# Performance work log

Hardware: AMD Instinct MI355X
Metric: run time of the kernel (lower is better)

## Reference

```python
import jax, jax.numpy as jnp
import numpy as np

B = 512      # streamlines (graphs in the batch)
L = 128      # points per streamline
M = L - 1    # edges per direction per streamline == conv output length
IN = 3       # 3-D coordinates
K = 5        # kNN neighbors (self included, as in PyG knn)
FOV = 5      # conv kernel; odd so conv out length == M, matching the batch vector
PAD = FOV // 2
NC = 2
EPS = 1e-5


def _bn(x, g, b, m, v):
    # inference-mode BatchNorm1d
    return (x - m) * jax.lax.rsqrt(v + EPS) * g + b


def setup_inputs():
    key = jax.random.key(0)
    ks = jax.random.split(key, 20)
    r = lambda i, shape: jax.random.normal(ks[i], shape, jnp.float32) * 0.05
    ones = lambda n: jnp.ones((n,), jnp.float32)
    zeros = lambda n: jnp.zeros((n,), jnp.float32)
    pos = jax.random.normal(ks[0], (B * L, IN), jnp.float32)
    # consecutive-point (forward) edges, streamline-major order
    base = (jnp.arange(B)[:, None] * L + jnp.arange(M)[None, :]).reshape(-1)
    fwd = jnp.stack([base, base + 1]).astype(jnp.int32)          # [2, B*M]
    eidx = jnp.concatenate([fwd, fwd], axis=1)                   # [2, 2*B*M]; first half overwritten in forward
    batch = jnp.repeat(jnp.arange(B, dtype=jnp.int32), L)        # per-point graph id
    lengths = jnp.full((B,), L, dtype=jnp.int32)
    return dict(
        pos=pos, eidx=eidx, batch=batch, lengths=lengths,
        conv1_w=r(1, (FOV, 2 * IN, 64)), conv1_b=r(2, (64,)),
        bn1_g=ones(64), bn1_b=zeros(64), bn1_m=r(3, (64,)), bn1_v=ones(64),
        edge_w=r(4, (2 * 64, 128)), edge_b=r(5, (128,)),
        bn2_g=ones(128), bn2_b=zeros(128), bn2_m=r(6, (128,)), bn2_v=ones(128),
        lin1_w=r(7, (64 + 128, 1024)), lin1_b=r(8, (1024,)),
        bn3_g=ones(1024), bn3_b=zeros(1024), bn3_m=r(9, (1024,)), bn3_v=ones(1024),
        m1_w=r(10, (1024, 512)), m1_b=r(11, (512,)),
        bn4_g=ones(512), bn4_b=zeros(512), bn4_m=r(12, (512,)), bn4_v=ones(512),
        m2_w=r(13, (512, 256)), m2_b=r(14, (256,)),
        bn5_g=ones(256), bn5_b=zeros(256), bn5_m=r(15, (256,)), bn5_v=ones(256),
        out_w=r(16, (256, NC)), out_b=r(17, (NC,)),
    )


def reference(pos, eidx, batch, lengths,
              conv1_w, conv1_b, bn1_g, bn1_b, bn1_m, bn1_v,
              edge_w, edge_b, bn2_g, bn2_b, bn2_m, bn2_v,
              lin1_w, lin1_b, bn3_g, bn3_b, bn3_m, bn3_v,
              m1_w, m1_b, bn4_g, bn4_b, bn4_m, bn4_v,
              m2_w, m2_b, bn5_g, bn5_b, bn5_m, bn5_v,
              out_w, out_b):
    E = eidx.shape[1]
    half = eidx[:, E // 2:]
    # eidx[:, :E//2] = eidx[:, E//2:].flip(1)
    eidx = jnp.concatenate([half[:, ::-1], half], axis=1)
    # irregular gather: edge features [E, 2*IN]
    feats = jnp.concatenate([pos[eidx[1]] - pos[eidx[0]], pos[eidx[0]]], axis=1)
    x = feats.reshape(2 * B, M, 2 * IN)                            # folded direction+batch
    # Conv1d (cross-correlation) -> BN -> ReLU, channels-last layout
    x = jax.lax.conv_general_dilated(x, conv1_w, (1,), [(PAD, PAD)],
                                     dimension_numbers=('NWC', 'WIO', 'NWC')) + conv1_b
    x = jax.nn.relu(_bn(x, bn1_g, bn1_b, bn1_m, bn1_v))            # [2B, M, 64]
    # direction symmetrization: max(first half, second half flipped on batch & length)
    x = jnp.maximum(x[:B], x[B:][::-1, ::-1, :])                   # [B, M, 64]
    x1 = x.reshape(B * M, 64)
    # ---- DynamicEdgeConv: per-streamline kNN graph + edge MLP + max aggregation ----
    xg = x1.reshape(B, M, 64)
    sq = jnp.sum(xg * xg, axis=-1)                                 # [B, M]
    dist = sq[:, :, None] + sq[:, None, :] - 2.0 * jnp.einsum('bmd,bnd->bmn', xg, xg)
    _, idx = jax.lax.top_k(-dist, K)                               # [B, M, K] (self included)
    xj = jax.vmap(lambda xs, ix: xs[ix])(xg, idx)                  # [B, M, K, 64]
    xi = jnp.broadcast_to(xg[:, :, None, :], xj.shape)
    ef = jnp.concatenate([xi, xj - xi], axis=-1)                   # [B, M, K, 128]
    ef = _bn(jax.nn.relu(ef @ edge_w + edge_b), bn2_g, bn2_b, bn2_m, bn2_v)
    x2 = jnp.max(ef, axis=2).reshape(B * M, 128)                   # max aggr over neighbors
    # ---- lin1 + global max pool + classifier MLP (dropout = identity in eval) ----
    h = jnp.concatenate([x1, x2], axis=1)                          # [N, 192]
    h = _bn(jax.nn.relu(h @ lin1_w + lin1_b), bn3_g, bn3_b, bn3_m, bn3_v)  # [N, 1024]
    g = jnp.max(h.reshape(B, M, 1024), axis=1)                     # global_max_pool -> [B, 1024]
    g = _bn(jax.nn.relu(g @ m1_w + m1_b), bn4_g, bn4_b, bn4_m, bn4_v)
    g = _bn(jax.nn.relu(g @ m2_w + m2_b), bn5_g, bn5_b, bn5_m, bn5_v)
    return g @ out_w + out_b                                       # [B, NC]
```

## Files before the change

kernel.cpp:

```cpp
#include <hip/hip_runtime.h>

#define BB 512
#define LL 128
#define MM 127
#define EPS 1e-5f

typedef _Float16 half4 __attribute__((ext_vector_type(4)));
typedef _Float16 half8 __attribute__((ext_vector_type(8)));
typedef float f32x16 __attribute__((ext_vector_type(16)));

#define HB_PITCH 384
#define HB_BATCH 49152

__global__ __launch_bounds__(256) void k0_prep(
    const float* __restrict__ lw, char* __restrict__ lwT,
    const float* __restrict__ ew, char* __restrict__ ewT,
    const float* __restrict__ m1w, char* __restrict__ m1wT,
    const float* __restrict__ m2w, char* __restrict__ m2wT)
{
  int tid = threadIdx.x;
  __shared__ float ws2[256][32];
  if (blockIdx.x < 32) {
    int c0 = blockIdx.x * 32;
    __shared__ float wcol[192][32];
    for (int i = tid; i < 192 * 32; i += 256) {
      int k = i >> 5, c = i & 31;
      wcol[k][c] = lw[k * 1024 + c0 + c];
    }
    __syncthreads();
    for (int j = tid; j < 768; j += 256) {
      int kg = j >> 5, c = j & 31;
      half8 v;
#pragma unroll
      for (int jj = 0; jj < 8; jj++) v[jj] = (_Float16)wcol[kg * 8 + jj][c];
      int cc = c0 + c;
      *(half8*)(lwT + cc * HB_PITCH + ((kg * 16) ^ ((cc & 7) << 4))) = v;
    }
  } else if (blockIdx.x == 32) {
    __shared__ float es[128][128];
    for (int i = tid; i < 128 * 128; i += 256) es[i >> 7][i & 127] = ew[i];
    __syncthreads();
    for (int i = tid; i < 256 * 8; i += 256) {
      int c = i >> 3, kg = i & 7;
      half8 v;
#pragma unroll
      for (int jj = 0; jj < 8; jj++) {
        int k = kg * 8 + jj;
        float val = (c < 128) ? (es[k][c] - es[64 + k][c]) : es[64 + k][c - 128];
        v[jj] = (_Float16)val;
      }
      *(half8*)(ewT + c * 128 + ((kg * 16) ^ ((c & 7) << 4))) = v;
    }
  } else {
    const float* src; char* dst; int N, K, c0, k0;
    if (blockIdx.x < 97) {
      int bb = blockIdx.x - 33;
      src = m1w; dst = m1wT; N = 512; K = 1024;
      c0 = (bb >> 2) * 32; k0 = (bb & 3) * 256;
    } else {
      int bb = blockIdx.x - 97;
      src = m2w; dst = m2wT; N = 256; K = 512;
      c0 = (bb >> 1) * 32; k0 = (bb & 1) * 256;
    }
    for (int i = tid; i < 256 * 32; i += 256) {
      int k = i >> 5, c = i & 31;
      ws2[k][c] = src[(size_t)(k0 + k) * N + c0 + c];
    }
    __syncthreads();
    for (int j = tid; j < 32 * 32; j += 256) {
      int kg = j >> 5, c = j & 31;
      half8 v;
#pragma unroll
      for (int jj = 0; jj < 8; jj++) v[jj] = (_Float16)ws2[kg * 8 + jj][c];
      int cc = c0 + c;
      *(half8*)(dst + (size_t)cc * (2 * K) + ((2 * (k0 + kg * 8)) ^ ((cc & 7) << 4))) = v;
    }
  }
}

__global__ __launch_bounds__(256, 1) void k1_conv_knn(
    const float* __restrict__ pos, const float* __restrict__ cw,
    const float* __restrict__ cb, const float* __restrict__ g1,
    const float* __restrict__ b1, const float* __restrict__ m1,
    const float* __restrict__ v1, char* __restrict__ hb,
    int* __restrict__ idxb)
{
  int b = blockIdx.x;
  int tid = threadIdx.x;
  __shared__ float ps[LL * 3];
  __shared__ float fpad[MM + 4][6];
  __shared__ float ws[5 * 6 * 64];
  __shared__ float s1s[64], t1s[64];
  __shared__ float xs[128][64];
  __shared__ float sq[128];
  __shared__ float S[128][132];
  __shared__ float bsl[2][128][5];
  __shared__ int   bil[2][128][5];

  for (int i = tid; i < LL * 3; i += 256) ps[i] = pos[b * LL * 3 + i];
  for (int i = tid; i < 5 * 6 * 64; i += 256) ws[i] = cw[i];
  if (tid < 64) {
    float s = g1[tid] * rsqrtf(v1[tid] + EPS);
    s1s[tid] = s;
    t1s[tid] = (cb[tid] - m1[tid]) * s + b1[tid];
  }
  if (tid < 24) {
    int r = tid / 6, c = tid % 6;
    int rr = (r < 2) ? r : (MM + r);
    fpad[rr][c] = 0.f;
  }
  if (tid < 64) xs[127][tid] = 0.f;
  __syncthreads();
  for (int i = tid; i < MM * 6; i += 256) {
    int m = i / 6, c = i % 6;
    float v = (c < 3) ? (ps[(m + 1) * 3 + c] - ps[m * 3 + c]) : ps[m * 3 + c - 3];
    fpad[m + 2][c] = v;
  }
  __syncthreads();
  int orow = BB - 1 - b;
  char* hbb = hb + (size_t)orow * HB_BATCH;
  if (tid < 8) *(float4*)(hbb + 127 * HB_PITCH + tid * 16) = make_float4(0.f, 0.f, 0.f, 0.f);
  for (int o = tid; o < MM * 64; o += 256) {
    int m = o >> 6, c = o & 63;
    float af = 0.f, ab = 0.f;
#pragma unroll
    for (int t = 0; t < 5; t++) {
#pragma unroll
      for (int ci = 0; ci < 6; ci++) {
        float wv = ws[(t * 6 + ci) * 64 + c];
        af = fmaf(fpad[m + t][ci], wv, af);
        ab = fmaf(fpad[m + 4 - t][ci], wv, ab);
      }
    }
    float z = fmaxf(af, ab) * s1s[c] + t1s[c];
    float xv = fmaxf(z, 0.f);
    int p = MM - 1 - m;
    xs[p][(((c >> 2) + (p >> 3)) & 15) * 4 + (c & 3)] = xv;
    *(_Float16*)(hbb + p * HB_PITCH + ((2 * c) ^ ((p & 7) << 4))) = (_Float16)xv;
  }
  __syncthreads();
  if (tid < 128) {
    int r = tid;
    float s = 0.f;
#pragma unroll
    for (int c4 = 0; c4 < 16; c4++) {
      float4 v = *(const float4*)&xs[r][((c4 + (r >> 3)) & 15) * 4];
      s = fmaf(v.x, v.x, s); s = fmaf(v.y, v.y, s);
      s = fmaf(v.z, v.z, s); s = fmaf(v.w, v.w, s);
    }
    sq[r] = s;
  }
  __syncthreads();
  {
    int tr = tid >> 4, tc = tid & 15;
    float acc[8][8];
#pragma unroll
    for (int i = 0; i < 8; i++)
#pragma unroll
      for (int j = 0; j < 8; j++) acc[i][j] = 0.f;
    for (int k4 = 0; k4 < 16; k4++) {
      int ca = ((k4 + tr) & 15) * 4;
      int cbo = ((k4 + tc) & 15) * 4;
      float4 av[8], bv[8];
#pragma unroll
      for (int i = 0; i < 8; i++) av[i] = *(const float4*)&xs[tr * 8 + i][ca];
#pragma unroll
      for (int j = 0; j < 8; j++) bv[j] = *(const float4*)&xs[tc * 8 + j][cbo];
#pragma unroll
      for (int i = 0; i < 8; i++)
#pragma unroll
        for (int j = 0; j < 8; j++) {
          acc[i][j] = fmaf(av[i].x, bv[j].x, acc[i][j]);
          acc[i][j] = fmaf(av[i].y, bv[j].y, acc[i][j]);
          acc[i][j] = fmaf(av[i].z, bv[j].z, acc[i][j]);
          acc[i][j] = fmaf(av[i].w, bv[j].w, acc[i][j]);
        }
    }
    float sqc[8];
#pragma unroll
    for (int j = 0; j < 8; j++) sqc[j] = sq[tc * 8 + j];
#pragma unroll
    for (int i = 0; i < 8; i++) {
      float4 s0, s1;
      s0.x = sqc[0] - 2.f * acc[i][0]; s0.y = sqc[1] - 2.f * acc[i][1];
      s0.z = sqc[2] - 2.f * acc[i][2]; s0.w = sqc[3] - 2.f * acc[i][3];
      s1.x = sqc[4] - 2.f * acc[i][4]; s1.y = sqc[5] - 2.f * acc[i][5];
      s1.z = sqc[6] - 2.f * acc[i][6]; s1.w = sqc[7] - 2.f * acc[i][7];
      *(float4*)&S[tr * 8 + i][tc * 8]     = s0;
      *(float4*)&S[tr * 8 + i][tc * 8 + 4] = s1;
    }
  }
  __syncthreads();
  {
    int row = tid & 127, half = tid >> 7;
    float bs[5]; int bi[5];
#pragma unroll
    for (int k = 0; k < 5; k++) { bs[k] = 1e30f; bi[k] = 0; }
    for (int q = 0; q < 16; q++) {
      float4 sv = *(const float4*)&S[row][half * 64 + q * 4];
      int cbase = half * 64 + q * 4;
      float va[4] = {sv.x, sv.y, sv.z, sv.w};
#pragma unroll
      for (int e = 0; e < 4; e++) {
        int col = cbase + e;
        float sc = va[e];
        if (col < 127 && sc < bs[4]) {
          bs[4] = sc; bi[4] = col;
#pragma unroll
          for (int k = 3; k >= 0; k--) {
            if (bs[k + 1] < bs[k]) {
              float ts = bs[k]; bs[k] = bs[k + 1]; bs[k + 1] = ts;
              int ti = bi[k]; bi[k] = bi[k + 1]; bi[k + 1] = ti;
            }
          }
        }
      }
    }
#pragma unroll
    for (int k = 0; k < 5; k++) { bsl[half][row][k] = bs[k]; bil[half][row][k] = bi[k]; }
  }
  __syncthreads();
  if (tid < MM) {
    int i0 = 0, i1 = 0;
    int base = (orow * MM + tid) * 5;
#pragma unroll
    for (int k = 0; k < 5; k++) {
      float v0 = bsl[0][tid][i0], v1 = bsl[1][tid][i1];
      int id;
      if (v0 <= v1) { id = bil[0][tid][i0]; i0++; }
      else          { id = bil[1][tid][i1]; i1++; }
      idxb[base + k] = id;
    }
  }
}

__global__ __launch_bounds__(256) void k3_edge(
    const int* __restrict__ idxb, const char* __restrict__ ewT,
    const float* __restrict__ eb, const float* __restrict__ g2,
    const float* __restrict__ b2, const float* __restrict__ m2,
    const float* __restrict__ v2, char* __restrict__ hb)
{
  int b = blockIdx.x;
  int tid = threadIdx.x;
  int w = tid >> 6, l = tid & 63;
  int lo = l & 31, hi = l >> 5;
  __shared__ _Float16 vvs[MM][136];
  __shared__ int idxs[MM * 5];
  char* hbb = hb + (size_t)b * HB_BATCH;

  for (int i = tid; i < MM * 5; i += 256) idxs[i] = idxb[b * MM * 5 + i];
  if (tid < 16) *(float4*)(hbb + 127 * HB_PITCH + 128 + tid * 16) = make_float4(0.f, 0.f, 0.f, 0.f);

  half8 af[4][4];
#pragma unroll
  for (int rt = 0; rt < 4; rt++) {
    int row = rt * 32 + lo;
    const char* rb = hbb + row * HB_PITCH;
    int sz = (row & 7) << 4;
#pragma unroll
    for (int ks = 0; ks < 4; ks++)
      af[rt][ks] = *(const half8*)(rb + ((ks * 32 + hi * 16) ^ sz));
  }
  int cu = w * 32 + lo;
  int swzW = (cu & 7) << 4;
  const char* wu = ewT + cu * 128;
  const char* wv = ewT + (128 + cu) * 128;
  half8 bu[4], bv[4];
#pragma unroll
  for (int ks = 0; ks < 4; ks++) {
    int off = (ks * 32 + hi * 16) ^ swzW;
    bu[ks] = *(const half8*)(wu + off);
    bv[ks] = *(const half8*)(wv + off);
  }
  f32x16 accu[4], accv[4];
#pragma unroll
  for (int rt = 0; rt < 4; rt++)
#pragma unroll
    for (int r = 0; r < 16; r++) { accu[rt][r] = 0.f; accv[rt][r] = 0.f; }
#pragma unroll
  for (int ks = 0; ks < 4; ks++)
#pragma unroll
    for (int rt = 0; rt < 4; rt++) {
      accu[rt] = __builtin_amdgcn_mfma_f32_32x32x16_f16(af[rt][ks], bu[ks], accu[rt], 0, 0, 0);
      accv[rt] = __builtin_amdgcn_mfma_f32_32x32x16_f16(af[rt][ks], bv[ks], accv[rt], 0, 0, 0);
    }
#pragma unroll
  for (int rt = 0; rt < 4; rt++)
#pragma unroll
    for (int r = 0; r < 16; r++) {
      int p = rt * 32 + (r & 3) + 8 * (r >> 2) + 4 * hi;
      if (p < MM) vvs[p][cu] = (_Float16)accv[rt][r];
    }
  __syncthreads();
  float ebv = eb[cu];
  float s2 = g2[cu] * rsqrtf(v2[cu] + EPS);
  float t2 = b2[cu] - m2[cu] * s2;
#pragma unroll
  for (int rt = 0; rt < 4; rt++)
#pragma unroll
    for (int r = 0; r < 16; r++) {
      int p = rt * 32 + (r & 3) + 8 * (r >> 2) + 4 * hi;
      if (p >= MM) continue;
      const int* ip = &idxs[p * 5];
      float u = accu[rt][r];
      float mx = -1e30f;
#pragma unroll
      for (int k = 0; k < 5; k++)
        mx = fmaxf(mx, u + (float)vvs[ip[k]][cu]);
      float o = fmaxf(mx + ebv, 0.f) * s2 + t2;
      *(_Float16*)(hbb + p * HB_PITCH + ((128 + 2 * cu) ^ ((p & 7) << 4))) = (_Float16)o;
    }
}

__global__ __launch_bounds__(512, 2) void k4_lin1(
    const char* __restrict__ hb, const char* __restrict__ lwT,
    const float* __restrict__ lb, const float* __restrict__ g3,
    const float* __restrict__ b3, const float* __restrict__ m3,
    const float* __restrict__ v3, char* __restrict__ gbufh)
{
  int b = blockIdx.x;
  int tid = threadIdx.x;
  int w = tid >> 6;
  int rh = w >> 2, cq = w & 3;
  int l = tid & 63;
  int lo = l & 31, hi = l >> 5;
  __shared__ __align__(16) char sA[HB_BATCH];
  __shared__ float rmslab[2][1024];

  {
    const char* gA = hb + (size_t)b * HB_BATCH;
#pragma unroll
    for (int i = 0; i < 6; i++)
      *(float4*)(sA + (i * 512 + tid) * 16) = *(const float4*)(gA + (i * 512 + tid) * 16);
  }
  __syncthreads();

  int sz = (lo & 7) << 4;
  half8 af[2][12];
#pragma unroll
  for (int q = 0; q < 2; q++) {
    const char* rbase = sA + ((rh * 2 + q) * 32 + lo) * HB_PITCH;
#pragma unroll
    for (int ks = 0; ks < 12; ks++)
      af[q][ks] = *(const half8*)(rbase + ((ks * 32 + hi * 16) ^ sz));
  }

  int col0 = cq * 256 + lo;
  half8 bf[2][12];
  {
    const char* cb0 = lwT + (size_t)col0 * HB_PITCH;
#pragma unroll
    for (int ks = 0; ks < 12; ks++)
      bf[0][ks] = *(const half8*)(cb0 + ((ks * 32 + hi * 16) ^ sz));
  }
#pragma unroll
  for (int ct = 0; ct < 8; ct++) {
    if (ct < 7) {
      const char* cbn = lwT + (size_t)(col0 + (ct + 1) * 32) * HB_PITCH;
#pragma unroll
      for (int ks = 0; ks < 12; ks++)
        bf[(ct + 1) & 1][ks] = *(const half8*)(cbn + ((ks * 32 + hi * 16) ^ sz));
    }
    f32x16 acc[2];
#pragma unroll
    for (int q = 0; q < 2; q++)
#pragma unroll
      for (int r = 0; r < 16; r++) acc[q][r] = 0.f;
#pragma unroll
    for (int ks = 0; ks < 12; ks++) {
      acc[0] = __builtin_amdgcn_mfma_f32_32x32x16_f16(af[0][ks], bf[ct & 1][ks], acc[0], 0, 0, 0);
      acc[1] = __builtin_amdgcn_mfma_f32_32x32x16_f16(af[1][ks], bf[ct & 1][ks], acc[1], 0, 0, 0);
    }
    int col = col0 + ct * 32;
    float bias = lb[col];
    float rm = 0.f;
#pragma unroll
    for (int q = 0; q < 2; q++)
#pragma unroll
      for (int r = 0; r < 16; r++) {
        float v = fmaxf(acc[q][r] + bias, 0.f);
        if (q == 1 && r == 15) v = (rh == 1 && hi == 1) ? 0.f : v;
        rm = fmaxf(rm, v);
      }
    rm = fmaxf(rm, __shfl_xor(rm, 32));
    if (hi == 0) rmslab[rh][col] = rm;
  }
  __syncthreads();
  if (tid < 256) {
    half4 o;
#pragma unroll
    for (int j = 0; j < 4; j++) {
      int c = tid * 4 + j;
      float mv = fmaxf(rmslab[0][c], rmslab[1][c]);
      float s = g3[c] * rsqrtf(v3[c] + EPS);
      float t = b3[c] - m3[c] * s;
      o[j] = (_Float16)(mv * s + t);
    }
    *(half4*)(gbufh + (size_t)b * 2048 + ((8 * tid) ^ ((b & 7) << 4))) = o;
  }
}

template<int K, int N>
__global__ __launch_bounds__(64) void k5_gemm(
    const char* __restrict__ inh, const char* __restrict__ wT,
    const float* __restrict__ bias, const float* __restrict__ gg,
    const float* __restrict__ bbp, const float* __restrict__ mmp,
    const float* __restrict__ vvp, char* __restrict__ outh,
    float* __restrict__ outf)
{
  constexpr int NT = N / 32;
  constexpr int NC = K / 128;
  int bid = blockIdx.x;
  int mt = bid / NT, nt = bid % NT;
  int l = threadIdx.x;
  int lo = l & 31, hi = l >> 5;
  int row = mt * 32 + lo, col = nt * 32 + lo;
  const char* arow = inh + (size_t)row * (2 * K);
  const char* brow = wT + (size_t)col * (2 * K);
  int sza = (row & 7) << 4, szb = (col & 7) << 4;

  half8 a[2][8], bf[2][8];
#pragma unroll
  for (int ks = 0; ks < 8; ks++) {
    int off = ks * 32 + hi * 16;
    a[0][ks]  = *(const half8*)(arow + (off ^ sza));
    bf[0][ks] = *(const half8*)(brow + (off ^ szb));
  }
  f32x16 acc;
#pragma unroll
  for (int r = 0; r < 16; r++) acc[r] = 0.f;
#pragma unroll
  for (int c = 0; c < NC; c++) {
    if (c + 1 < NC) {
#pragma unroll
      for (int ks = 0; ks < 8; ks++) {
        int off = (c + 1) * 256 + ks * 32 + hi * 16;
        a[(c + 1) & 1][ks]  = *(const half8*)(arow + (off ^ sza));
        bf[(c + 1) & 1][ks] = *(const half8*)(brow + (off ^ szb));
      }
    }
#pragma unroll
    for (int ks = 0; ks < 8; ks++)
      acc = __builtin_amdgcn_mfma_f32_32x32x16_f16(a[c & 1][ks], bf[c & 1][ks], acc, 0, 0, 0);
  }
  float bv = bias[col];
  float s = gg[col] * rsqrtf(vvp[col] + EPS);
  float t = bbp[col] - mmp[col] * s;
#pragma unroll
  for (int r = 0; r < 16; r++) {
    float z = fmaxf(acc[r] + bv, 0.f) * s + t;
    int orow = mt * 32 + (r & 3) + 8 * (r >> 2) + 4 * hi;
    if (outh)
      *(_Float16*)(outh + (size_t)orow * (2 * N) + ((2 * col) ^ ((orow & 7) << 4))) = (_Float16)z;
    else
      outf[(size_t)orow * N + col] = z;
  }
}

__global__ __launch_bounds__(256) void k5c_out(
    const float* __restrict__ c2, const float* __restrict__ ow,
    const float* __restrict__ ob, float* __restrict__ out)
{
  int t = blockIdx.x * 256 + threadIdx.x;
  int r = t >> 1, c = t & 1;
  float acc = 0.f;
  for (int d4 = 0; d4 < 64; d4++) {
    float4 cv = *(const float4*)(c2 + r * 256 + d4 * 4);
    acc = fmaf(cv.x, ow[(d4 * 4 + 0) * 2 + c], acc);
    acc = fmaf(cv.y, ow[(d4 * 4 + 1) * 2 + c], acc);
    acc = fmaf(cv.z, ow[(d4 * 4 + 2) * 2 + c], acc);
    acc = fmaf(cv.w, ow[(d4 * 4 + 3) * 2 + c], acc);
  }
  out[t] = acc + ob[c];
}

extern "C" void kernel_launch(void* const* d_in, const int* in_sizes, int n_in,
                              void* d_out, int out_size, void* d_ws, size_t ws_size,
                              hipStream_t stream)
{
  const float* pos = (const float*)d_in[0];
  const float* cw  = (const float*)d_in[4];
  const float* cb  = (const float*)d_in[5];
  const float* g1  = (const float*)d_in[6];
  const float* b1  = (const float*)d_in[7];
  const float* m1  = (const float*)d_in[8];
  const float* v1  = (const float*)d_in[9];
  const float* ew  = (const float*)d_in[10];
  const float* eb  = (const float*)d_in[11];
  const float* g2  = (const float*)d_in[12];
  const float* b2  = (const float*)d_in[13];
  const float* m2  = (const float*)d_in[14];
  const float* v2  = (const float*)d_in[15];
  const float* lw  = (const float*)d_in[16];
  const float* lb  = (const float*)d_in[17];
  const float* g3  = (const float*)d_in[18];
  const float* b3  = (const float*)d_in[19];
  const float* m3  = (const float*)d_in[20];
  const float* v3  = (const float*)d_in[21];
  const float* m1w = (const float*)d_in[22];
  const float* m1b = (const float*)d_in[23];
  const float* g4  = (const float*)d_in[24];
  const float* b4  = (const float*)d_in[25];
  const float* m4  = (const float*)d_in[26];
  const float* v4  = (const float*)d_in[27];
  const float* m2w = (const float*)d_in[28];
  const float* m2b = (const float*)d_in[29];
  const float* g5  = (const float*)d_in[30];
  const float* b5  = (const float*)d_in[31];
  const float* m5  = (const float*)d_in[32];
  const float* v5  = (const float*)d_in[33];
  const float* ow  = (const float*)d_in[34];
  const float* ob  = (const float*)d_in[35];

  char* ws = (char*)d_ws;
  char*  hb    = ws;
  char*  lwT   = ws + 25165824;
  char*  ewT   = ws + 25559040;
  int*   idxb  = (int*)(ws + 25591808);
  char*  gbufh = ws + 26892288;
  char*  m1wT  = ws + 27940864;
  char*  c1h   = ws + 28989440;
  char*  m2wT  = ws + 29513728;
  float* c2    = (float*)(ws + 29775872);

  hipLaunchKernelGGL(k0_prep, dim3(113), dim3(256), 0, stream,
                     lw, lwT, ew, ewT, m1w, m1wT, m2w, m2wT);
  hipLaunchKernelGGL(k1_conv_knn, dim3(512), dim3(256), 0, stream,
                     pos, cw, cb, g1, b1, m1, v1, hb, idxb);
  hipLaunchKernelGGL(k3_edge, dim3(512), dim3(256), 0, stream,
                     idxb, ewT, eb, g2, b2, m2, v2, hb);
  hipLaunchKernelGGL(k4_lin1, dim3(512), dim3(512), 0, stream,
                     hb, lwT, lb, g3, b3, m3, v3, gbufh);
  (k5_gemm<1024, 512>)<<<dim3(256), dim3(64), 0, stream>>>(
      gbufh, m1wT, m1b, g4, b4, m4, v4, c1h, nullptr);
  (k5_gemm<512, 256>)<<<dim3(128), dim3(64), 0, stream>>>(
      c1h, m2wT, m2b, g5, b5, m5, v5, nullptr, c2);
  hipLaunchKernelGGL(k5c_out, dim3(4), dim3(256), 0, stream,
                     c2, ow, ob, (float*)d_out);
}
```

Baseline: 140.3 us.

## Widen conv+kNN kernel to 512 threads with register weights and 4-way top-k

The conv+kNN kernel now runs 512 threads per block (launch bound 512, 2). Conv weights and BN scale/shift are held in registers instead of shared memory, and each thread computes 4 output rows from float4-loaded padded input. The top-k scan splits each row across 4 quarter-threads with a 4-way merge. This aims to raise parallelism and occupancy in k1 and shorten its serial phases, at the cost of register pressure and half the threads sitting idle during the distance GEMM.

Result: faster. 128.3 us (-8.5%).

```diff
diff --git a/kernel.cpp b/kernel.cpp
--- a/kernel.cpp
+++ b/kernel.cpp
@@ -78,7 +78,7 @@
   }
 }
 
-__global__ __launch_bounds__(256, 1) void k1_conv_knn(
+__global__ __launch_bounds__(512, 2) void k1_conv_knn(
     const float* __restrict__ pos, const float* __restrict__ cw,
     const float* __restrict__ cb, const float* __restrict__ g1,
     const float* __restrict__ b1, const float* __restrict__ m1,
@@ -87,56 +87,72 @@
 {
   int b = blockIdx.x;
   int tid = threadIdx.x;
-  __shared__ float ps[LL * 3];
-  __shared__ float fpad[MM + 4][6];
-  __shared__ float ws[5 * 6 * 64];
-  __shared__ float s1s[64], t1s[64];
+  __shared__ float fpad[132][8];
   __shared__ float xs[128][64];
   __shared__ float sq[128];
   __shared__ float S[128][132];
-  __shared__ float bsl[2][128][5];
-  __shared__ int   bil[2][128][5];
-
-  for (int i = tid; i < LL * 3; i += 256) ps[i] = pos[b * LL * 3 + i];
-  for (int i = tid; i < 5 * 6 * 64; i += 256) ws[i] = cw[i];
-  if (tid < 64) {
-    float s = g1[tid] * rsqrtf(v1[tid] + EPS);
-    s1s[tid] = s;
-    t1s[tid] = (cb[tid] - m1[tid]) * s + b1[tid];
-  }
-  if (tid < 24) {
-    int r = tid / 6, c = tid % 6;
-    int rr = (r < 2) ? r : (MM + r);
-    fpad[rr][c] = 0.f;
+  __shared__ float bsl[4][128][5];
+  __shared__ int   bil[4][128][5];
+
+  if (tid < 40) {
+    int rr = tid >> 3;
+    int row = (rr < 2) ? rr : (127 + rr);
+    fpad[row][tid & 7] = 0.f;
   }
   if (tid < 64) xs[127][tid] = 0.f;
-  __syncthreads();
-  for (int i = tid; i < MM * 6; i += 256) {
+  const float* pb = pos + b * LL * 3;
+  for (int i = tid; i < MM * 6; i += 512) {
     int m = i / 6, c = i % 6;
-    float v = (c < 3) ? (ps[(m + 1) * 3 + c] - ps[m * 3 + c]) : ps[m * 3 + c - 3];
+    float v = (c < 3) ? (pb[(m + 1) * 3 + c] - pb[m * 3 + c]) : pb[m * 3 + c - 3];
     fpad[m + 2][c] = v;
   }
-  __syncthreads();
   int orow = BB - 1 - b;
   char* hbb = hb + (size_t)orow * HB_BATCH;
   if (tid < 8) *(float4*)(hbb + 127 * HB_PITCH + tid * 16) = make_float4(0.f, 0.f, 0.f, 0.f);
-  for (int o = tid; o < MM * 64; o += 256) {
-    int m = o >> 6, c = o & 63;
-    float af = 0.f, ab = 0.f;
-#pragma unroll
-    for (int t = 0; t < 5; t++) {
-#pragma unroll
-      for (int ci = 0; ci < 6; ci++) {
-        float wv = ws[(t * 6 + ci) * 64 + c];
-        af = fmaf(fpad[m + t][ci], wv, af);
-        ab = fmaf(fpad[m + 4 - t][ci], wv, ab);
+
+  int c = tid & 63, cg = tid >> 6;
+  float wreg[30];
+#pragma unroll
+  for (int t = 0; t < 5; t++)
+#pragma unroll
+    for (int ci = 0; ci < 6; ci++) wreg[t * 6 + ci] = cw[(t * 6 + ci) * 64 + c];
+  float s1 = g1[c] * rsqrtf(v1[c] + EPS);
+  float t1 = (cb[c] - m1[c]) * s1 + b1[c];
+  __syncthreads();
+
+#pragma unroll
+  for (int it = 0; it < 4; it++) {
+    int chunk = cg + 8 * it;
+    int m0 = chunk * 4;
+    float4 fa[8], fb[8];
+#pragma unroll
+    for (int r = 0; r < 8; r++) {
+      fa[r] = *(const float4*)&fpad[m0 + r][0];
+      fb[r] = *(const float4*)&fpad[m0 + r][4];
+    }
+#pragma unroll
+    for (int mm = 0; mm < 4; mm++) {
+      int m = m0 + mm;
+      if (m >= MM) continue;
+      float af = 0.f, ab = 0.f;
+#pragma unroll
+      for (int t = 0; t < 5; t++) {
+#pragma unroll
+        for (int ci = 0; ci < 6; ci++) {
+          float w = wreg[t * 6 + ci];
+          int rf = mm + t, rb = mm + 4 - t;
+          float xf = (ci < 4) ? ((const float*)&fa[rf])[ci] : ((const float*)&fb[rf])[ci - 4];
+          float xb = (ci < 4) ? ((const float*)&fa[rb])[ci] : ((const float*)&fb[rb])[ci - 4];
+          af = fmaf(xf, w, af);
+          ab = fmaf(xb, w, ab);
+        }
       }
-    }
-    float z = fmaxf(af, ab) * s1s[c] + t1s[c];
-    float xv = fmaxf(z, 0.f);
-    int p = MM - 1 - m;
-    xs[p][(((c >> 2) + (p >> 3)) & 15) * 4 + (c & 3)] = xv;
-    *(_Float16*)(hbb + p * HB_PITCH + ((2 * c) ^ ((p & 7) << 4))) = (_Float16)xv;
+      float z = fmaxf(af, ab) * s1 + t1;
+      float xv = fmaxf(z, 0.f);
+      int p = MM - 1 - m;
+      xs[p][(((c >> 2) + (p >> 3)) & 15) * 4 + (c & 3)] = xv;
+      *(_Float16*)(hbb + p * HB_PITCH + ((2 * c) ^ ((p & 7) << 4))) = (_Float16)xv;
+    }
   }
   __syncthreads();
   if (tid < 128) {
@@ -151,7 +167,7 @@
     sq[r] = s;
   }
   __syncthreads();
-  {
+  if (tid < 256) {
     int tr = tid >> 4, tc = tid & 15;
     float acc[8][8];
 #pragma unroll
@@ -181,24 +197,25 @@
     for (int j = 0; j < 8; j++) sqc[j] = sq[tc * 8 + j];
 #pragma unroll
     for (int i = 0; i < 8; i++) {
-      float4 s0, s1;
+      float4 s0, s1v;
       s0.x = sqc[0] - 2.f * acc[i][0]; s0.y = sqc[1] - 2.f * acc[i][1];
       s0.z = sqc[2] - 2.f * acc[i][2]; s0.w = sqc[3] - 2.f * acc[i][3];
-      s1.x = sqc[4] - 2.f * acc[i][4]; s1.y = sqc[5] - 2.f * acc[i][5];
-      s1.z = sqc[6] - 2.f * acc[i][6]; s1.w = sqc[7] - 2.f * acc[i][7];
+      s1v.x = sqc[4] - 2.f * acc[i][4]; s1v.y = sqc[5] - 2.f * acc[i][5];
+      s1v.z = sqc[6] - 2.f * acc[i][6]; s1v.w = sqc[7] - 2.f * acc[i][7];
       *(float4*)&S[tr * 8 + i][tc * 8]     = s0;
-      *(float4*)&S[tr * 8 + i][tc * 8 + 4] = s1;
+      *(float4*)&S[tr * 8 + i][tc * 8 + 4] = s1v;
     }
   }
   __syncthreads();
   {
-    int row = tid & 127, half = tid >> 7;
+    int row = tid & 127, q = tid >> 7;
     float bs[5]; int bi[5];
 #pragma unroll
     for (int k = 0; k < 5; k++) { bs[k] = 1e30f; bi[k] = 0; }
-    for (int q = 0; q < 16; q++) {
-      float4 sv = *(const float4*)&S[row][half * 64 + q * 4];
-      int cbase = half * 64 + q * 4;
+#pragma unroll
+    for (int e4 = 0; e4 < 8; e4++) {
+      float4 sv = *(const float4*)&S[row][q * 32 + e4 * 4];
+      int cbase = q * 32 + e4 * 4;
       float va[4] = {sv.x, sv.y, sv.z, sv.w};
 #pragma unroll
       for (int e = 0; e < 4; e++) {
@@ -217,19 +234,23 @@
       }
     }
 #pragma unroll
-    for (int k = 0; k < 5; k++) { bsl[half][row][k] = bs[k]; bil[half][row][k] = bi[k]; }
+    for (int k = 0; k < 5; k++) { bsl[q][row][k] = bs[k]; bil[q][row][k] = bi[k]; }
   }
   __syncthreads();
   if (tid < MM) {
-    int i0 = 0, i1 = 0;
+    int i0 = 0, i1 = 0, i2 = 0, i3 = 0;
     int base = (orow * MM + tid) * 5;
 #pragma unroll
     for (int k = 0; k < 5; k++) {
       float v0 = bsl[0][tid][i0], v1 = bsl[1][tid][i1];
-      int id;
-      if (v0 <= v1) { id = bil[0][tid][i0]; i0++; }
-      else          { id = bil[1][tid][i1]; i1++; }
-      idxb[base + k] = id;
+      float v2 = bsl[2][tid][i2], v3 = bsl[3][tid][i3];
+      float best = v0; int q = 0;
+      if (v1 < best) { best = v1; q = 1; }
+      if (v2 < best) { best = v2; q = 2; }
+      if (v3 < best) { best = v3; q = 3; }
+      int iq = (q == 0) ? i0 : (q == 1) ? i1 : (q == 2) ? i2 : i3;
+      idxb[base + k] = bil[q][tid][iq];
+      if (q == 0) i0++; else if (q == 1) i1++; else if (q == 2) i2++; else i3++;
     }
   }
 }
@@ -525,7 +546,7 @@
 
   hipLaunchKernelGGL(k0_prep, dim3(113), dim3(256), 0, stream,
                      lw, lwT, ew, ewT, m1w, m1wT, m2w, m2wT);
-  hipLaunchKernelGGL(k1_conv_knn, dim3(512), dim3(256), 0, stream,
+  hipLaunchKernelGGL(k1_conv_knn, dim3(512), dim3(512), 0, stream,
                      pos, cw, cb, g1, b1, m1, v1, hb, idxb);
   hipLaunchKernelGGL(k3_edge, dim3(512), dim3(256), 0, stream,
                      idxb, ewT, eb, g2, b2, m2, v2, hb);
```
